# Kernel tuning notes

Measured on AMD Instinct MI355X. Metric: run time of the kernel, lower is better.

## Reference

```python
import jax, jax.numpy as jnp
import numpy as np

H = 2048          # hidden_size
HEAD = 64         # head_size
NH = H // HEAD    # n_heads = 32
B, T = 4, 4096
LORA_MIX = 32     # per-branch rank of time_maa low-rank mixer (5 branches)
LORA_DECAY = 64   # rank of decay low-rank mixer


def setup_inputs() -> dict:
    key = jax.random.key(0)
    ks = jax.random.split(key, 24)
    s = 0.02  # small init scale keeps tanh/silu in sane range
    inp = {
        "hidden": jax.random.normal(ks[0], (B, T, H), jnp.float32),
        "attn_x": jax.random.normal(ks[1], (B, H), jnp.float32),
        "attn_kv": jax.random.normal(ks[2], (B, NH, HEAD, HEAD), jnp.float32),
        "ffn_x": jax.random.normal(ks[3], (B, H), jnp.float32),
        "time_maa_x": jax.random.normal(ks[4], (1, 1, H), jnp.float32) * s,
        "time_maa_w": jax.random.normal(ks[5], (1, 1, H), jnp.float32) * s,
        "time_maa_k": jax.random.normal(ks[6], (1, 1, H), jnp.float32) * s,
        "time_maa_v": jax.random.normal(ks[7], (1, 1, H), jnp.float32) * s,
        "time_maa_r": jax.random.normal(ks[8], (1, 1, H), jnp.float32) * s,
        "time_maa_g": jax.random.normal(ks[9], (1, 1, H), jnp.float32) * s,
        "time_maa_w1": jax.random.normal(ks[10], (H, LORA_MIX * 5), jnp.float32) * s,
        "time_maa_w2": jax.random.normal(ks[11], (5, LORA_MIX, H), jnp.float32) * s,
        "time_decay": jax.random.normal(ks[12], (1, 1, H), jnp.float32) * s,
        "time_decay_w1": jax.random.normal(ks[13], (H, LORA_DECAY), jnp.float32) * s,
        "time_decay_w2": jax.random.normal(ks[14], (LORA_DECAY, H), jnp.float32) * s,
        "time_faaaa": jax.random.normal(ks[15], (NH, HEAD), jnp.float32) * s,
        "receptance_w": jax.random.normal(ks[16], (H, H), jnp.float32) * s,
        "key_w": jax.random.normal(ks[17], (H, H), jnp.float32) * s,
        "value_w": jax.random.normal(ks[18], (H, H), jnp.float32) * s,
        "gate_w": jax.random.normal(ks[19], (H, H), jnp.float32) * s,
        "output_w": jax.random.normal(ks[20], (H, H), jnp.float32) * s,
    }
    return inp


def reference(hidden, attn_x, attn_kv, ffn_x,
              time_maa_x, time_maa_w, time_maa_k, time_maa_v, time_maa_r, time_maa_g,
              time_maa_w1, time_maa_w2,
              time_decay, time_decay_w1, time_decay_w2, time_faaaa,
              receptance_w, key_w, value_w, gate_w, output_w):
    b, t, h = hidden.shape
    # token shift: prepend previous chunk's last token state
    shifted = jnp.concatenate([attn_x[:, None, :], hidden[:, :-1, :]], axis=1)  # [B,T,H]
    x = hidden
    xx = shifted - x
    # low-rank data-dependent mixing coefficients (5 branches)
    xxx = x + xx * time_maa_x                                        # [B,T,H]
    xxx = jnp.tanh(xxx.reshape(-1, h) @ time_maa_w1)                 # [B*T, 5*32]
    xxx = xxx.reshape(-1, 5, LORA_MIX).transpose(1, 0, 2)            # [5, B*T, 32]
    xxx = jnp.einsum('fnr,frh->fnh', xxx, time_maa_w2)               # [5, B*T, H]
    xxx = xxx.reshape(5, b, t, h)
    mw, mk, mv, mr, mg = xxx[0], xxx[1], xxx[2], xxx[3], xxx[4]
    # note: source uses additive mix (x + xx + coeff), faithful to code as written
    td_in = x + xx + (time_maa_w + mw)
    k_in = x + xx + (time_maa_k + mk)
    v_in = x + xx + (time_maa_v + mv)
    r_in = x + xx + (time_maa_r + mr)
    g_in = x + xx + (time_maa_g + mg)
    receptance = jnp.einsum('bth,hd->btd', r_in, receptance_w)
    key = jnp.einsum('bth,hd->btd', k_in, key_w)
    value = jnp.einsum('bth,hd->btd', v_in, value_w)
    gate = jax.nn.silu(jnp.einsum('bth,hd->btd', g_in, gate_w))
    td = jnp.tanh(jnp.einsum('bth,hr->btr', td_in, time_decay_w1))
    td = jnp.einsum('btr,rh->bth', td, time_decay_w2)
    td = time_decay + td                                              # [B,T,H] per-channel decay
    attn_x_new = hidden[:, -1]                                        # [B,H]
    return (receptance, key, value, gate, td, attn_x_new)
```

## Files before the change

### kernel.cpp

```cpp
#include <hip/hip_runtime.h>

#define H 2048
#define TT 4096
#define BB 4
#define NROWS (BB * TT)
#define NTH ((size_t)NROWS * H)
#define KCAT (H + 32)
#define KC8  (H + 64)
#define NTH64 ((size_t)NROWS * 64)

typedef __attribute__((ext_vector_type(8))) short bh8;
typedef __attribute__((ext_vector_type(4))) float f32x4;

__device__ inline unsigned short f2bf(float f) {
    union { float f; unsigned u; } v; v.f = f;
    unsigned r = v.u + 0x7fff + ((v.u >> 16) & 1);
    return (unsigned short)(r >> 16);
}
__device__ inline float bf2f(unsigned short u) {
    union { unsigned u; float f; } v; v.u = ((unsigned)u) << 16; return v.f;
}
__device__ inline void gload_lds16(const void* g, void* l) {
    __builtin_amdgcn_global_load_lds(
        (const __attribute__((address_space(1))) void*)g,
        (__attribute__((address_space(3))) void*)l, 16, 0, 0);
}

__global__ __launch_bounds__(256) void prep_kernel(
    const float* __restrict__ hidden, const float* __restrict__ attn_x,
    const float* __restrict__ tmx,
    unsigned short* __restrict__ shifted, unsigned short* __restrict__ xin,
    float* __restrict__ out5) {
    size_t i = ((size_t)blockIdx.x * 256 + threadIdx.x) * 4;
    int n = (int)(i >> 11);
    int h = (int)(i & 2047);
    int t = n & (TT - 1);
    float4 x = *(const float4*)(hidden + i);
    float4 s;
    if (t == 0) {
        int b = n >> 12;
        s = *(const float4*)(attn_x + ((size_t)b << 11) + h);
    } else {
        s = *(const float4*)(hidden + (i - H));
    }
    float4 m = *(const float4*)(tmx + h);
    ushort4 sh, xi;
    sh.x = f2bf(s.x); sh.y = f2bf(s.y); sh.z = f2bf(s.z); sh.w = f2bf(s.w);
    xi.x = f2bf(x.x + (s.x - x.x) * m.x);
    xi.y = f2bf(x.y + (s.y - x.y) * m.y);
    xi.z = f2bf(x.z + (s.z - x.z) * m.z);
    xi.w = f2bf(x.w + (s.w - x.w) * m.w);
    *(ushort4*)(shifted + i) = sh;
    *(ushort4*)(xin + i) = xi;
    if (t == TT - 1) {
        int b = n >> 12;
        *(float4*)(out5 + ((size_t)b << 11) + h) = x;
    }
}

__global__ __launch_bounds__(256) void transpose_kernel(
    const float* __restrict__ in, unsigned short* __restrict__ outp,
    int R, int C, int ldo) {
    __shared__ float tile[32][33];
    int tx = threadIdx.x & 31, ty = threadIdx.x >> 5;
    int r0 = blockIdx.y * 32, c0 = blockIdx.x * 32;
    for (int i = ty; i < 32; i += 8) {
        int r = r0 + i, c = c0 + tx;
        tile[i][tx] = (r < R && c < C) ? in[(size_t)r * C + c] : 0.f;
    }
    __syncthreads();
    for (int i = ty; i < 32; i += 8) {
        int c = c0 + i, r = r0 + tx;
        if (c < C && r < R) outp[(size_t)c * ldo + r] = f2bf(tile[tx][i]);
    }
}

__global__ __launch_bounds__(256) void transpose4_kernel(
    const float* __restrict__ w0, const float* __restrict__ w1,
    const float* __restrict__ w2, const float* __restrict__ w3,
    unsigned short* __restrict__ d0, unsigned short* __restrict__ d1,
    unsigned short* __restrict__ d2, unsigned short* __restrict__ d3) {
    __shared__ float tile[32][33];
    int bz = blockIdx.z;
    const float* in = bz == 0 ? w0 : bz == 1 ? w1 : bz == 2 ? w2 : w3;
    unsigned short* outp = bz == 0 ? d0 : bz == 1 ? d1 : bz == 2 ? d2 : d3;
    int tx = threadIdx.x & 31, ty = threadIdx.x >> 5;
    int r0 = blockIdx.y * 32, c0 = blockIdx.x * 32;
    for (int i = ty; i < 32; i += 8)
        tile[i][tx] = in[(size_t)(r0 + i) * H + c0 + tx];
    __syncthreads();
    for (int i = ty; i < 32; i += 8)
        outp[(size_t)(c0 + i) * KC8 + r0 + tx] = f2bf(tile[tx][i]);
}

__global__ __launch_bounds__(256) void w2wp_kernel(
    const float* __restrict__ W2,
    const float* __restrict__ w0, const float* __restrict__ w1,
    const float* __restrict__ w2, const float* __restrict__ w3,
    const float* __restrict__ W1d,
    float* __restrict__ part) {
    const int br = blockIdx.z, ks = blockIdx.y, dblk = blockIdx.x;
    const int tid = threadIdx.x;
    const float* W; int D;
    if (br < 4) { W = br == 0 ? w0 : br == 1 ? w1 : br == 2 ? w2 : w3; D = H; }
    else        { W = W1d; D = 64; }
    const int f = br < 4 ? ((0x4213 >> (br * 4)) & 15) : 0;
    const float* W2f = W2 + (size_t)f * 32 * H;
    __shared__ float w2s[256][32];
    const int k0 = ks * 256;
    for (int idx = tid; idx < 8192; idx += 256) {
        int r = idx & 31, kk = idx >> 5;
        w2s[kk][r] = W2f[(size_t)r * H + k0 + kk];
    }
    __syncthreads();
    int d = dblk * 256 + tid;
    if (d >= D) return;
    float a[32];
#pragma unroll
    for (int r = 0; r < 32; ++r) a[r] = 0.f;
    for (int kk = 0; kk < 256; ++kk) {
        float w = W[(size_t)(k0 + kk) * D + d];
        const float4* w4 = (const float4*)w2s[kk];
#pragma unroll
        for (int rq = 0; rq < 8; ++rq) {
            float4 v = w4[rq];
            a[rq * 4 + 0] += v.x * w;
            a[rq * 4 + 1] += v.y * w;
            a[rq * 4 + 2] += v.z * w;
            a[rq * 4 + 3] += v.w * w;
        }
    }
    float* pp = part + (((size_t)br * 8 + ks) * 32) * 2048 + d;
#pragma unroll
    for (int r = 0; r < 32; ++r) pp[(size_t)r * 2048] = a[r];
}

__global__ __launch_bounds__(256) void w2wr_kernel(
    const float* __restrict__ part,
    unsigned short* __restrict__ dR, unsigned short* __restrict__ dK,
    unsigned short* __restrict__ dV, unsigned short* __restrict__ dG,
    unsigned short* __restrict__ d1) {
    int gid = blockIdx.x * 256 + threadIdx.x;
    if (gid < 262144) {
        int br = gid >> 16, rem = gid & 65535;
        int r = rem >> 11, d = rem & 2047;
        float s = 0.f;
#pragma unroll
        for (int ks = 0; ks < 8; ++ks)
            s += part[(((size_t)br * 8 + ks) * 32 + r) * 2048 + d];
        unsigned short* dst = br == 0 ? dR : br == 1 ? dK : br == 2 ? dV : dG;
        dst[(size_t)d * KC8 + H + r] = f2bf(s);
        dst[(size_t)d * KC8 + H + 32 + r] = 0;
    } else {
        int q = gid - 262144;
        int r = q >> 6, d = q & 63;
        float s = 0.f;
#pragma unroll
        for (int ks = 0; ks < 8; ++ks)
            s += part[(((size_t)4 * 8 + ks) * 32 + r) * 2048 + d];
        d1[(size_t)d * KCAT + H + r] = f2bf(s);
    }
}

__global__ __launch_bounds__(256) void bias_all_kernel(
    const unsigned short* __restrict__ bR, const unsigned short* __restrict__ bK,
    const unsigned short* __restrict__ bV, const unsigned short* __restrict__ bG,
    const unsigned short* __restrict__ b1,
    const float* __restrict__ mR, const float* __restrict__ mK,
    const float* __restrict__ mV, const float* __restrict__ mG,
    const float* __restrict__ mW,
    float* __restrict__ bias4, float* __restrict__ bias0) {
    int wave = threadIdx.x >> 6, lane = threadIdx.x & 63;
    int p = blockIdx.x * 4 + wave;
    const unsigned short* src; const float* maa; float* dst;
    if (p < 8192) {
        int br = p >> 11, row = p & 2047;
        src = (br == 0 ? bR : br == 1 ? bK : br == 2 ? bV : bG) + (size_t)row * KC8;
        maa = (br == 0 ? mR : br == 1 ? mK : br == 2 ? mV : mG);
        dst = bias4 + br * H + row;
    } else {
        int q = p - 8192;
        if (q >= 64) return;
        src = b1 + (size_t)q * KCAT; maa = mW; dst = bias0 + q;
    }
    float a = 0.f;
#pragma unroll 4
    for (int i = 0; i < 32; ++i) { int h = i * 64 + lane; a += bf2f(src[h]) * maa[h]; }
    for (int s = 32; s; s >>= 1) a += __shfl_xor(a, s);
    if (lane == 0) *dst = a;
}

template <int WM, int WN, int FM, int FN, int HAS_BIAS, int ACT, int OF32, int ZPAD>
__global__ __launch_bounds__(256) void gemm_kernel(
    const unsigned short* __restrict__ A, int lda,
    const unsigned short* __restrict__ A2, int lda2, int KS,
    const unsigned short* __restrict__ Bt, int ldb, int K,
    void* __restrict__ outp, int ldo, int NT,
    const float* __restrict__ bias) {
    static_assert(WM * WN == 4, "4 waves");
    constexpr int BM = WM * FM * 16;
    constexpr int BN = WN * FN * 16;
    __shared__ unsigned short As[BM * 32];
    __shared__ unsigned short Bs[BN * 32];

    const int nb = gridDim.x;
    const int bid = blockIdx.x;
    const int swz = (bid & 7) * (nb >> 3) + (bid >> 3);
    const int mt = swz / NT, nt = swz % NT;
    const int m0 = mt * BM, n0 = nt * BN;

    const int tid = threadIdx.x;
    const int wave = tid >> 6, lane = tid & 63;
    const int l16 = lane & 15, kh = lane >> 4;
    const int wr = wave / WN, wc = wave % WN;

    f32x4 acc[FM][FN] = {};

    constexpr int ACH = BM * 4;
    constexpr int BCH = BN * 4;

    for (int k0 = 0; k0 < K; k0 += 32) {
#pragma unroll
        for (int i = 0; i < (ACH + 255) / 256; ++i) {
            int c = i * 256 + tid;
            if (ACH % 256 == 0 || c < ACH) {
                int row = c >> 2, ck = c & 3;
                int kk = k0 + ck * 8;
                const unsigned short* gp = (kk < KS)
                    ? A  + (size_t)(m0 + row) * lda  + kk
                    : A2 + (size_t)(m0 + row) * lda2 + (kk - KS);
                gload_lds16(gp, As + (size_t)(i * 256 + wave * 64) * 8);
            }
        }
#pragma unroll
        for (int i = 0; i < (BCH + 255) / 256; ++i) {
            int c = i * 256 + tid;
            if (BCH % 256 == 0 || c < BCH) {
                int row = c >> 2, ck = c & 3;
                gload_lds16(Bt + (size_t)(n0 + row) * ldb + k0 + ck * 8,
                            Bs + (size_t)(i * 256 + wave * 64) * 8);
            }
        }
        __syncthreads();
        bh8 av[FM], bv[FN];
#pragma unroll
        for (int mi = 0; mi < FM; ++mi)
            av[mi] = *(const bh8*)((const char*)As + (((wr * FM + mi) * 16 + l16) * 64 + kh * 16));
#pragma unroll
        for (int ni = 0; ni < FN; ++ni)
            bv[ni] = *(const bh8*)((const char*)Bs + (((wc * FN + ni) * 16 + l16) * 64 + kh * 16));
#pragma unroll
        for (int mi = 0; mi < FM; ++mi)
#pragma unroll
            for (int ni = 0; ni < FN; ++ni)
                acc[mi][ni] = __builtin_amdgcn_mfma_f32_16x16x32_bf16(
                    av[mi], bv[ni], acc[mi][ni], 0, 0, 0);
        __syncthreads();
    }

#pragma unroll
    for (int mi = 0; mi < FM; ++mi) {
#pragma unroll
        for (int ni = 0; ni < FN; ++ni) {
            int col = n0 + (wc * FN + ni) * 16 + l16;
            float bcol = HAS_BIAS ? bias[col] : 0.f;
#pragma unroll
            for (int j = 0; j < 4; ++j) {
                int row = m0 + (wr * FM + mi) * 16 + kh * 4 + j;
                float v = acc[mi][ni][j] + bcol;
                if (ACT == 1) v = v * (1.f / (1.f + __expf(-v)));
                else if (ACT == 2) v = tanhf(v);
                if (ZPAD) {
                    int br = col >> 5, cc = col & 31;
                    unsigned short* zp = (unsigned short*)outp
                        + (size_t)br * NTH64 + (size_t)row * 64 + cc;
                    zp[0] = f2bf(v);
                    zp[32] = 0;
                } else if (OF32) {
                    ((float*)outp)[(size_t)row * ldo + col] = v;
                } else {
                    ((unsigned short*)outp)[(size_t)row * ldo + col] = f2bf(v);
                }
            }
        }
    }
}

__global__ __launch_bounds__(512, 2) void bigproj8_kernel(
    const unsigned short* __restrict__ A,
    const unsigned short* __restrict__ zpad,
    const unsigned short* __restrict__ bt0, const unsigned short* __restrict__ bt1,
    const unsigned short* __restrict__ bt2, const unsigned short* __restrict__ bt3,
    const float* __restrict__ bias4, float* __restrict__ out) {
    constexpr int BUFB = 32768;
    constexpr int NTK = KC8 / 32;
    __shared__ alignas(16) char lds[4 * BUFB];

    const int bid = blockIdx.x;
    const int swz = (bid & 7) * 256 + (bid >> 3);
    const int branch = swz >> 9;
    const int tile = swz & 511;
    const int m0 = (tile >> 3) * 256, n0 = (tile & 7) * 256;

    const unsigned short* Bt = branch == 0 ? bt0 : branch == 1 ? bt1
                             : branch == 2 ? bt2 : bt3;
    const int f = (0x4213 >> (branch * 4)) & 15;
    const unsigned short* Az = zpad + (size_t)f * NTH64;

    const int tid = threadIdx.x;
    const int wave = tid >> 6, lane = tid & 63;
    const int l16 = lane & 15, kh = lane >> 4;
    const int wm = wave >> 2, wn = wave & 3;
    const int kh16 = kh * 16;
    const int swr = (l16 & 8) << 2;

    const int rS = tid >> 2;
    const int kbx = ((tid & 3) * 16) ^ ((rS & 8) << 2);
    const char* bA0 = (const char*)A  + (size_t)(m0 + rS) * 4096 + kbx;
    const char* bA1 = bA0 + (size_t)128 * 4096;
    const char* bz0 = (const char*)Az + (size_t)(m0 + rS) * 128 + kbx;
    const char* bz1 = bz0 + (size_t)128 * 128;
    const char* bB0 = (const char*)Bt + (size_t)(n0 + rS) * (KC8 * 2) + kbx;
    const char* bB1 = bB0 + (size_t)128 * (KC8 * 2);
    const int dA0 = wave * 1024, dA1 = 8192 + wave * 1024;

    auto stageA = [&](int kt, char* nb) {
        const char *p0, *p1;
        if (kt < 64) { size_t o = (size_t)kt * 64;        p0 = bA0 + o; p1 = bA1 + o; }
        else         { size_t o = (size_t)(kt - 64) * 64; p0 = bz0 + o; p1 = bz1 + o; }
        gload_lds16(p0, nb + dA0);
        gload_lds16(p1, nb + dA1);
    };
    auto stageB = [&](int kt, char* nb) {
        size_t o = (size_t)kt * 64;
        gload_lds16(bB0 + o, nb + 16384 + dA0);
        gload_lds16(bB1 + o, nb + 16384 + dA1);
    };

    f32x4 acc[8][4] = {};
    bh8 avlo[4], avhi[4], bvA[4], bvB[4];

    stageA(0, lds);        stageB(0, lds);
    stageA(1, lds + BUFB); stageB(1, lds + BUFB);
    asm volatile("s_waitcnt vmcnt(4)" ::: "memory");
    __builtin_amdgcn_s_barrier();
    __builtin_amdgcn_sched_barrier(0);
#pragma unroll
    for (int i = 0; i < 4; ++i) {
        avlo[i] = *(const bh8*)(lds + (wm * 8 + i) * 1024 + l16 * 64 + (kh16 ^ swr));
        bvA[i]  = *(const bh8*)(lds + 16384 + (wn * 4 + i) * 1024 + l16 * 64 + (kh16 ^ swr));
    }

    auto tile_step = [&](int t, bh8 (&bvC)[4], bh8 (&bvN)[4]) {
        const char* Ab = lds + (t & 3) * BUFB;
        char* nb = lds + ((t + 2) & 3) * BUFB;
        const bool doSt = (t + 2) < NTK;

#pragma unroll
        for (int i = 0; i < 4; ++i)
            avhi[i] = *(const bh8*)(Ab + (wm * 8 + 4 + i) * 1024 + l16 * 64 + (kh16 ^ swr));
        if (doSt) stageA(t + 2, nb);
        __builtin_amdgcn_s_setprio(1);
#pragma unroll
        for (int mi = 0; mi < 4; ++mi)
#pragma unroll
            for (int ni = 0; ni < 4; ++ni)
                acc[mi][ni] = __builtin_amdgcn_mfma_f32_16x16x32_bf16(
                    avlo[mi], bvC[ni], acc[mi][ni], 0, 0, 0);
        __builtin_amdgcn_s_setprio(0);

        if (doSt) stageB(t + 2, nb);
        if (t + 1 < NTK) {
            if (doSt) asm volatile("s_waitcnt vmcnt(4)" ::: "memory");
            else      asm volatile("s_waitcnt vmcnt(0)" ::: "memory");
            __builtin_amdgcn_s_barrier();
            __builtin_amdgcn_sched_barrier(0);
            const char* Ab1 = lds + ((t + 1) & 3) * BUFB;
#pragma unroll
            for (int i = 0; i < 4; ++i) {
                avlo[i] = *(const bh8*)(Ab1 + (wm * 8 + i) * 1024 + l16 * 64 + (kh16 ^ swr));
                bvN[i]  = *(const bh8*)(Ab1 + 16384 + (wn * 4 + i) * 1024 + l16 * 64 + (kh16 ^ swr));
            }
        }
        __builtin_amdgcn_s_setprio(1);
#pragma unroll
        for (int mi = 0; mi < 4; ++mi)
#pragma unroll
            for (int ni = 0; ni < 4; ++ni)
                acc[4 + mi][ni] = __builtin_amdgcn_mfma_f32_16x16x32_bf16(
                    avhi[mi], bvC[ni], acc[4 + mi][ni], 0, 0, 0);
        __builtin_amdgcn_s_setprio(0);
    };

    for (int t = 0; t < NTK; t += 2) {
        tile_step(t,     bvA, bvB);
        tile_step(t + 1, bvB, bvA);
    }

    float* outp = out + (size_t)branch * NTH;
    const float* bias = bias4 + branch * H;
#pragma unroll
    for (int a = 0; a < 8; ++a) {
#pragma unroll
        for (int b = 0; b < 4; ++b) {
            int col = n0 + wn * 64 + b * 16 + l16;
            float bc = bias[col];
#pragma unroll
            for (int j = 0; j < 4; ++j) {
                int row = m0 + wm * 128 + a * 16 + kh * 4 + j;
                float v = acc[a][b][j] + bc;
                if (branch == 3) v = v * (1.f / (1.f + __expf(-v)));
                outp[(size_t)row * H + col] = v;
            }
        }
    }
}

__global__ __launch_bounds__(256) void td2_kernel(
    const float* __restrict__ tdmid, const float* __restrict__ W2d,
    const float* __restrict__ tdecay, float* __restrict__ outp) {
    int col = blockIdx.x * 256 + threadIdx.x;
    int row0 = blockIdx.y * 8;
    float a[8] = {0, 0, 0, 0, 0, 0, 0, 0};
    for (int r = 0; r < 64; ++r) {
        float w = W2d[(size_t)r * H + col];
#pragma unroll
        for (int j = 0; j < 8; ++j)
            a[j] += tdmid[(size_t)(row0 + j) * 64 + r] * w;
    }
    float b = tdecay[col];
#pragma unroll
    for (int j = 0; j < 8; ++j)
        outp[(size_t)(row0 + j) * H + col] = a[j] + b;
}

extern "C" void kernel_launch(void* const* d_in, const int* in_sizes, int n_in,
                              void* d_out, int out_size, void* d_ws, size_t ws_size,
                              hipStream_t stream) {
    const float* hidden = (const float*)d_in[0];
    const float* attn_x = (const float*)d_in[1];
    const float* tmx    = (const float*)d_in[4];
    const float* tmaa_w = (const float*)d_in[5];
    const float* tmaa_k = (const float*)d_in[6];
    const float* tmaa_v = (const float*)d_in[7];
    const float* tmaa_r = (const float*)d_in[8];
    const float* tmaa_g = (const float*)d_in[9];
    const float* W1     = (const float*)d_in[10];
    const float* W2     = (const float*)d_in[11];
    const float* tdecay = (const float*)d_in[12];
    const float* W1d    = (const float*)d_in[13];
    const float* W2d    = (const float*)d_in[14];
    const float* Wr     = (const float*)d_in[16];
    const float* Wk     = (const float*)d_in[17];
    const float* Wv     = (const float*)d_in[18];
    const float* Wg     = (const float*)d_in[19];

    float* out = (float*)d_out;

    char* ws = (char*)d_ws;
    size_t off = 0;
    auto alloc = [&](size_t bytes) {
        char* p = ws + off;
        off = (off + bytes + 255) & ~(size_t)255;
        return p;
    };
    unsigned short* shifted = (unsigned short*)alloc(NTH * 2);
    unsigned short* xin     = (unsigned short*)alloc(NTH * 2);
    unsigned short* zpad    = (unsigned short*)alloc(5 * NTH64 * 2);
    unsigned short* W1t     = (unsigned short*)alloc((size_t)160 * H * 2);
    unsigned short* BcatR   = (unsigned short*)alloc((size_t)H * KC8 * 2);
    unsigned short* BcatK   = (unsigned short*)alloc((size_t)H * KC8 * 2);
    unsigned short* BcatV   = (unsigned short*)alloc((size_t)H * KC8 * 2);
    unsigned short* BcatG   = (unsigned short*)alloc((size_t)H * KC8 * 2);
    unsigned short* Bcat1   = (unsigned short*)alloc((size_t)64 * KCAT * 2);
    float* tdmid            = (float*)alloc((size_t)NROWS * 64 * 4);
    float* part             = (float*)alloc((size_t)5 * 8 * 32 * 2048 * 4);
    float* bias4            = (float*)alloc(4 * H * 4);
    float* bias0            = (float*)alloc(64 * 4);

    prep_kernel<<<(unsigned)(NTH / (4 * 256)), 256, 0, stream>>>(
        hidden, attn_x, tmx, shifted, xin, out + 5 * NTH);

    transpose4_kernel<<<dim3(64, 64, 4), 256, 0, stream>>>(
        Wr, Wk, Wv, Wg, BcatR, BcatK, BcatV, BcatG);
    transpose_kernel<<<dim3(5, 64), 256, 0, stream>>>(W1, W1t, H, 160, H);
    transpose_kernel<<<dim3(2, 64), 256, 0, stream>>>(W1d, Bcat1, H, 64, KCAT);
    w2wp_kernel<<<dim3(8, 8, 5), 256, 0, stream>>>(
        W2, Wr, Wk, Wv, Wg, W1d, part);
    w2wr_kernel<<<1032, 256, 0, stream>>>(
        part, BcatR, BcatK, BcatV, BcatG, Bcat1);
    bias_all_kernel<<<2064, 256, 0, stream>>>(
        BcatR, BcatK, BcatV, BcatG, Bcat1,
        tmaa_r, tmaa_k, tmaa_v, tmaa_g, tmaa_w, bias4, bias0);

    gemm_kernel<4, 1, 1, 10, 0, 2, 0, 1><<<256, 256, 0, stream>>>(
        xin, H, xin, H, H, W1t, H, H, zpad, 0, 1, nullptr);

    bigproj8_kernel<<<2048, 512, 0, stream>>>(
        shifted, zpad, BcatR, BcatK, BcatV, BcatG, bias4, out);

    gemm_kernel<4, 1, 1, 4, 1, 2, 1, 0><<<256, 256, 0, stream>>>(
        shifted, H, zpad, 64, H, Bcat1, KCAT, KCAT,
        tdmid, 64, 1, bias0);
    td2_kernel<<<dim3(8, NROWS / 8), 256, 0, stream>>>(
        tdmid, W2d, tdecay, out + 4 * NTH);
}
```

Measured before the change: 883.9 us.

## Fold bias computation into W2 fold kernel and merge decay GEMM into bigproj

The maa-vector bias is now computed as a 33rd accumulator row in the W2·W fold kernel and reduced in w2wr, which removes the separate bias_all kernel. The decay low-rank GEMM (tanh of shifted·W1d plus bias) is folded into the bigproj8 launch as 128 extra leading blocks, which removes one launch and lets it overlap with the large projection. The cost is extra register pressure from a 33-wide accumulator, and bigproj blocks that are lightly loaded at 512 threads with a simple unpipelined loop. The bias is now accumulated in fp32 before bf16 rounding, which slightly changes numerics.

```diff
diff --git a/kernel.cpp b/kernel.cpp
--- a/kernel.cpp
+++ b/kernel.cpp
@@ -98,48 +98,47 @@
     const float* __restrict__ w0, const float* __restrict__ w1,
     const float* __restrict__ w2, const float* __restrict__ w3,
     const float* __restrict__ W1d,
+    const float* __restrict__ mR, const float* __restrict__ mK,
+    const float* __restrict__ mV, const float* __restrict__ mG,
+    const float* __restrict__ mW,
     float* __restrict__ part) {
     const int br = blockIdx.z, ks = blockIdx.y, dblk = blockIdx.x;
     const int tid = threadIdx.x;
-    const float* W; int D;
-    if (br < 4) { W = br == 0 ? w0 : br == 1 ? w1 : br == 2 ? w2 : w3; D = H; }
-    else        { W = W1d; D = 64; }
+    const float* W; int D; const float* maa;
+    if (br < 4) {
+        W = br == 0 ? w0 : br == 1 ? w1 : br == 2 ? w2 : w3; D = H;
+        maa = br == 0 ? mR : br == 1 ? mK : br == 2 ? mV : mG;
+    } else { W = W1d; D = 64; maa = mW; }
     const int f = br < 4 ? ((0x4213 >> (br * 4)) & 15) : 0;
     const float* W2f = W2 + (size_t)f * 32 * H;
-    __shared__ float w2s[256][32];
+    __shared__ float w2s[256][33];
     const int k0 = ks * 256;
-    for (int idx = tid; idx < 8192; idx += 256) {
-        int r = idx & 31, kk = idx >> 5;
-        w2s[kk][r] = W2f[(size_t)r * H + k0 + kk];
-    }
+#pragma unroll
+    for (int r = 0; r < 33; ++r)
+        w2s[tid][r] = (r < 32) ? W2f[(size_t)r * H + k0 + tid] : maa[k0 + tid];
     __syncthreads();
     int d = dblk * 256 + tid;
     if (d >= D) return;
-    float a[32];
-#pragma unroll
-    for (int r = 0; r < 32; ++r) a[r] = 0.f;
+    float a[33];
+#pragma unroll
+    for (int r = 0; r < 33; ++r) a[r] = 0.f;
     for (int kk = 0; kk < 256; ++kk) {
         float w = W[(size_t)(k0 + kk) * D + d];
-        const float4* w4 = (const float4*)w2s[kk];
-#pragma unroll
-        for (int rq = 0; rq < 8; ++rq) {
-            float4 v = w4[rq];
-            a[rq * 4 + 0] += v.x * w;
-            a[rq * 4 + 1] += v.y * w;
-            a[rq * 4 + 2] += v.z * w;
-            a[rq * 4 + 3] += v.w * w;
-        }
-    }
-    float* pp = part + (((size_t)br * 8 + ks) * 32) * 2048 + d;
-#pragma unroll
-    for (int r = 0; r < 32; ++r) pp[(size_t)r * 2048] = a[r];
+        const float* ws2 = w2s[kk];
+#pragma unroll
+        for (int r = 0; r < 33; ++r) a[r] += ws2[r] * w;
+    }
+    float* pp = part + (((size_t)br * 8 + ks) * 33) * 2048 + d;
+#pragma unroll
+    for (int r = 0; r < 33; ++r) pp[(size_t)r * 2048] = a[r];
 }
 
 __global__ __launch_bounds__(256) void w2wr_kernel(
     const float* __restrict__ part,
     unsigned short* __restrict__ dR, unsigned short* __restrict__ dK,
     unsigned short* __restrict__ dV, unsigned short* __restrict__ dG,
-    unsigned short* __restrict__ d1) {
+    unsigned short* __restrict__ d1,
+    float* __restrict__ bias4, float* __restrict__ bias0) {
     int gid = blockIdx.x * 256 + threadIdx.x;
     if (gid < 262144) {
         int br = gid >> 16, rem = gid & 65535;
@@ -147,47 +146,34 @@
         float s = 0.f;
 #pragma unroll
         for (int ks = 0; ks < 8; ++ks)
-            s += part[(((size_t)br * 8 + ks) * 32 + r) * 2048 + d];
+            s += part[(((size_t)br * 8 + ks) * 33 + r) * 2048 + d];
         unsigned short* dst = br == 0 ? dR : br == 1 ? dK : br == 2 ? dV : dG;
         dst[(size_t)d * KC8 + H + r] = f2bf(s);
         dst[(size_t)d * KC8 + H + 32 + r] = 0;
-    } else {
+    } else if (gid < 264192) {
         int q = gid - 262144;
         int r = q >> 6, d = q & 63;
         float s = 0.f;
 #pragma unroll
         for (int ks = 0; ks < 8; ++ks)
-            s += part[(((size_t)4 * 8 + ks) * 32 + r) * 2048 + d];
+            s += part[(((size_t)4 * 8 + ks) * 33 + r) * 2048 + d];
         d1[(size_t)d * KCAT + H + r] = f2bf(s);
-    }
-}
-
-__global__ __launch_bounds__(256) void bias_all_kernel(
-    const unsigned short* __restrict__ bR, const unsigned short* __restrict__ bK,
-    const unsigned short* __restrict__ bV, const unsigned short* __restrict__ bG,
-    const unsigned short* __restrict__ b1,
-    const float* __restrict__ mR, const float* __restrict__ mK,
-    const float* __restrict__ mV, const float* __restrict__ mG,
-    const float* __restrict__ mW,
-    float* __restrict__ bias4, float* __restrict__ bias0) {
-    int wave = threadIdx.x >> 6, lane = threadIdx.x & 63;
-    int p = blockIdx.x * 4 + wave;
-    const unsigned short* src; const float* maa; float* dst;
-    if (p < 8192) {
-        int br = p >> 11, row = p & 2047;
-        src = (br == 0 ? bR : br == 1 ? bK : br == 2 ? bV : bG) + (size_t)row * KC8;
-        maa = (br == 0 ? mR : br == 1 ? mK : br == 2 ? mV : mG);
-        dst = bias4 + br * H + row;
-    } else {
-        int q = p - 8192;
-        if (q >= 64) return;
-        src = b1 + (size_t)q * KCAT; maa = mW; dst = bias0 + q;
-    }
-    float a = 0.f;
-#pragma unroll 4
-    for (int i = 0; i < 32; ++i) { int h = i * 64 + lane; a += bf2f(src[h]) * maa[h]; }
-    for (int s = 32; s; s >>= 1) a += __shfl_xor(a, s);
-    if (lane == 0) *dst = a;
+    } else if (gid < 272384) {
+        int q = gid - 264192;
+        int br = q >> 11, d = q & 2047;
+        float s = 0.f;
+#pragma unroll
+        for (int ks = 0; ks < 8; ++ks)
+            s += part[(((size_t)br * 8 + ks) * 33 + 32) * 2048 + d];
+        bias4[br * H + d] = s;
+    } else if (gid < 272448) {
+        int d = gid - 272384;
+        float s = 0.f;
+#pragma unroll
+        for (int ks = 0; ks < 8; ++ks)
+            s += part[(((size_t)4 * 8 + ks) * 33 + 32) * 2048 + d];
+        bias0[d] = s;
+    }
 }
 
 template <int WM, int WN, int FM, int FN, int HAS_BIAS, int ACT, int OF32, int ZPAD>
@@ -291,12 +277,59 @@
     const unsigned short* __restrict__ zpad,
     const unsigned short* __restrict__ bt0, const unsigned short* __restrict__ bt1,
     const unsigned short* __restrict__ bt2, const unsigned short* __restrict__ bt3,
-    const float* __restrict__ bias4, float* __restrict__ out) {
+    const unsigned short* __restrict__ Bcat1,
+    const float* __restrict__ bias4, const float* __restrict__ bias0,
+    float* __restrict__ out, float* __restrict__ tdmid) {
     constexpr int BUFB = 32768;
     constexpr int NTK = KC8 / 32;
     __shared__ alignas(16) char lds[4 * BUFB];
 
-    const int bid = blockIdx.x;
+    const int tid = threadIdx.x;
+    const int wave = tid >> 6, lane = tid & 63;
+    const int l16 = lane & 15, kh = lane >> 4;
+    const int kh16 = kh * 16;
+
+    if (blockIdx.x < 128) {
+        unsigned short* As = (unsigned short*)lds;
+        unsigned short* Bs = (unsigned short*)(lds + 8192);
+        const int m0 = blockIdx.x * 128;
+        f32x4 acc[4] = {};
+        const int rowS = tid >> 2, ckS = tid & 3;
+        for (int k0 = 0; k0 < KCAT; k0 += 32) {
+            {
+                int kk = k0 + ckS * 8;
+                const unsigned short* gp = (kk < H)
+                    ? A    + (size_t)(m0 + rowS) * H + kk
+                    : zpad + (size_t)(m0 + rowS) * 64 + (kk - H);
+                gload_lds16(gp, As + (size_t)(wave * 64) * 8);
+            }
+            if (tid < 256) {
+                gload_lds16(Bcat1 + (size_t)rowS * KCAT + k0 + ckS * 8,
+                            Bs + (size_t)(wave * 64) * 8);
+            }
+            __syncthreads();
+            bh8 av = *(const bh8*)((const char*)As + ((wave * 16 + l16) * 64 + kh16));
+#pragma unroll
+            for (int ni = 0; ni < 4; ++ni) {
+                bh8 bv = *(const bh8*)((const char*)Bs + ((ni * 16 + l16) * 64 + kh16));
+                acc[ni] = __builtin_amdgcn_mfma_f32_16x16x32_bf16(av, bv, acc[ni], 0, 0, 0);
+            }
+            __syncthreads();
+        }
+#pragma unroll
+        for (int ni = 0; ni < 4; ++ni) {
+            int col = ni * 16 + l16;
+            float bc = bias0[col];
+#pragma unroll
+            for (int j = 0; j < 4; ++j) {
+                int row = m0 + wave * 16 + kh * 4 + j;
+                tdmid[(size_t)row * 64 + col] = tanhf(acc[ni][j] + bc);
+            }
+        }
+        return;
+    }
+
+    const int bid = blockIdx.x - 128;
     const int swz = (bid & 7) * 256 + (bid >> 3);
     const int branch = swz >> 9;
     const int tile = swz & 511;
@@ -307,11 +340,7 @@
     const int f = (0x4213 >> (branch * 4)) & 15;
     const unsigned short* Az = zpad + (size_t)f * NTH64;
 
-    const int tid = threadIdx.x;
-    const int wave = tid >> 6, lane = tid & 63;
-    const int l16 = lane & 15, kh = lane >> 4;
     const int wm = wave >> 2, wn = wave & 3;
-    const int kh16 = kh * 16;
     const int swr = (l16 & 8) << 2;
 
     const int rS = tid >> 2;
@@ -474,7 +503,7 @@
     unsigned short* BcatG   = (unsigned short*)alloc((size_t)H * KC8 * 2);
     unsigned short* Bcat1   = (unsigned short*)alloc((size_t)64 * KCAT * 2);
     float* tdmid            = (float*)alloc((size_t)NROWS * 64 * 4);
-    float* part             = (float*)alloc((size_t)5 * 8 * 32 * 2048 * 4);
+    float* part             = (float*)alloc((size_t)5 * 8 * 33 * 2048 * 4);
     float* bias4            = (float*)alloc(4 * H * 4);
     float* bias0            = (float*)alloc(64 * 4);
 
@@ -486,22 +515,18 @@
     transpose_kernel<<<dim3(5, 64), 256, 0, stream>>>(W1, W1t, H, 160, H);
     transpose_kernel<<<dim3(2, 64), 256, 0, stream>>>(W1d, Bcat1, H, 64, KCAT);
     w2wp_kernel<<<dim3(8, 8, 5), 256, 0, stream>>>(
-        W2, Wr, Wk, Wv, Wg, W1d, part);
-    w2wr_kernel<<<1032, 256, 0, stream>>>(
-        part, BcatR, BcatK, BcatV, BcatG, Bcat1);
-    bias_all_kernel<<<2064, 256, 0, stream>>>(
-        BcatR, BcatK, BcatV, BcatG, Bcat1,
-        tmaa_r, tmaa_k, tmaa_v, tmaa_g, tmaa_w, bias4, bias0);
+        W2, Wr, Wk, Wv, Wg, W1d,
+        tmaa_r, tmaa_k, tmaa_v, tmaa_g, tmaa_w, part);
+    w2wr_kernel<<<1065, 256, 0, stream>>>(
+        part, BcatR, BcatK, BcatV, BcatG, Bcat1, bias4, bias0);
 
     gemm_kernel<4, 1, 1, 10, 0, 2, 0, 1><<<256, 256, 0, stream>>>(
         xin, H, xin, H, H, W1t, H, H, zpad, 0, 1, nullptr);
 
-    bigproj8_kernel<<<2048, 512, 0, stream>>>(
-        shifted, zpad, BcatR, BcatK, BcatV, BcatG, bias4, out);
-
-    gemm_kernel<4, 1, 1, 4, 1, 2, 1, 0><<<256, 256, 0, stream>>>(
-        shifted, H, zpad, 64, H, Bcat1, KCAT, KCAT,
-        tdmid, 64, 1, bias0);
+    bigproj8_kernel<<<2176, 512, 0, stream>>>(
+        shifted, zpad, BcatR, BcatK, BcatV, BcatG, Bcat1,
+        bias4, bias0, out, tdmid);
+
     td2_kernel<<<dim3(8, NROWS / 8), 256, 0, stream>>>(
         tdmid, W2d, tdecay, out + 4 * NTH);
 }
```

Result: faster. 853.6 us (-3.4%).
